# Performance work log

Hardware: AMD Instinct MI355X
Metric: run time of the kernel (lower is better)

The kernel has to match this reference:

```python
import jax, jax.numpy as jnp
import numpy as np

B, T, H = 512, 32, 300


def setup_inputs() -> dict:
    key = jax.random.key(0)
    ks = jax.random.split(key, 24)
    u = lambda k, shape: jax.random.uniform(k, shape, jnp.float32, -0.1, 0.1)
    return {
        'local_inputs': jax.random.normal(ks[0], (B, T, 28, 10), jnp.float32),
        'labels': jax.random.normal(ks[1], (B, T, 1, 1), jnp.float32),
        'extras': jax.random.normal(ks[2], (B, T, 4, 1), jnp.float32),
        'DisM': jax.random.normal(ks[3], (10,), jnp.float32),
        'AngleM': jax.random.uniform(ks[4], (10,), jnp.float32, 0.0, 360.0),
        'Wih': u(ks[5], (10, 4 * H, 11)),
        'b_ih': u(ks[6], (10, 4 * H)),
        'b_hh': u(ks[7], (10, 4 * H)),
        'Wt': u(ks[8], (4 * H, 4)),
        'bt_ih': u(ks[9], (4 * H,)),
        'bt_hh': u(ks[10], (4 * H,)),
        'wp': u(ks[11], (H, 2 * H)),
        'bp': u(ks[12], (H, 1)),
        'F1': u(ks[13], (2 * H, 200)),
        'b1': u(ks[14], (200,)),
        'F2': u(ks[15], (202, 1)),
        'b2': u(ks[16], (1,)),
        'ff': u(ks[17], (100, 17)),
        'bff': u(ks[18], (100, 1)),
        'fuse1': u(ks[19], (H, 100)),
        'biasf': u(ks[20], (100,)),
        'Wout': u(ks[21], (100, 1)),
        'biasout': u(ks[22], (1,)),
        'a': u(ks[23], (1,)),
    }


def reference(local_inputs, labels, extras, DisM, AngleM,
              Wih, b_ih, b_hh, Wt, bt_ih, bt_hh,
              wp, bp, F1, b1, F2, b2, ff, bff,
              fuse1, biasf, Wout, biasout, a):
    x = jnp.transpose(local_inputs, (1, 0, 2, 3))   # [T,B,28,10]
    exs = jnp.transpose(extras, (1, 0, 2, 3))       # [T,B,4,1]
    labels_r = jnp.transpose(labels, (1, 0, 2, 3)).reshape(T, B, 1)
    b_cells = b_ih + b_hh                            # weight_hh * 0 vanishes; biases remain
    bt = bt_ih + bt_hh
    wA = jax.nn.softmax(DisM)                        # [10] static distance weights
    aa = a[0]

    def cells(s):  # s: [B,11,10] -> con [B,H,10]; zero-state LSTMCell per neighbor
        g = jnp.einsum('kgi,bik->bkg', Wih, s) + b_cells  # [B,10,4H]
        i, f, gg, o = jnp.split(g, 4, axis=-1)
        h = jax.nn.sigmoid(o) * jnp.tanh(jax.nn.sigmoid(i) * jnp.tanh(gg))
        return jnp.transpose(h, (0, 2, 1))

    def target_cell(t):  # [B,4] -> [B,H]
        g = t @ Wt.T + bt
        i, f, gg, o = jnp.split(g, 4, axis=-1)
        return jax.nn.sigmoid(o) * jnp.tanh(jax.nn.sigmoid(i) * jnp.tanh(gg))

    def attend_predict(fl, con1, htarget):
        # fl: [B,28,10], con1: [B,H,10]
        hcat = jnp.concatenate([jnp.transpose(con1, (0, 2, 1)),
                                jnp.broadcast_to(htarget[:, None, :], (B, 10, H))], axis=2)  # [B,10,2H]
        fc1 = jax.nn.relu(jnp.einsum('bkh,ho->bko', hcat, F1) + b1)          # [B,10,200]
        ang = jnp.abs(fl[:, 10, :] - AngleM[None, :]) / 360.0                # [B,10]
        fc2 = jnp.concatenate([fc1, fl[:, 8, :, None], ang[..., None]], axis=2)  # [B,10,202]
        wdyn = jax.nn.relu(jnp.einsum('bko,od->bkd', fc2, F2)[..., 0] + b2[0])   # [B,10]
        # faithful to the original: softmax over neighbors of [10,B], then FLAT reshape to [B,1,10]
        wa3 = jax.nn.softmax(wdyn.T, axis=0).reshape(B, 1, 10)
        cat = jnp.sum(con1 * wa3, axis=2)                                    # [B,H]
        flin2 = jnp.einsum('of,bfk->bok', ff, fl[:, 11:, :]) + bff           # [B,100,10]
        fusiondis = jnp.sum(flin2 * wA[None, None, :], axis=2)               # [B,100]
        fuse = cat @ fuse1 + biasf                                           # [B,100]
        return (aa * fuse + (1.0 - aa) * fusiondis) @ Wout + biasout         # [B,1]

    # t = 0: con1 = con (no lastcon yet)
    con0 = cells(x[0, :, :11, :])
    p0 = attend_predict(x[0], con0, target_cell(exs[0, :, :4, 0]))

    def step(lastcon, inp):
        fl, e = inp
        con = cells(fl[:, :11, :])
        ht = target_cell(e[:, :4, 0])
        con1 = jax.nn.relu(jnp.einsum('oh,bhk->bok', wp,
                                      jnp.concatenate([con, lastcon], axis=1)) + bp)  # [B,H,10]
        return con, attend_predict(fl, con1, ht)

    _, preds = jax.lax.scan(step, con0, (x[1:], exs[1:]))
    preds = jnp.concatenate([p0[None], preds], axis=0)  # [T,B,1]
    return preds, labels_r
```

## Files before the change

kernel.cpp:

```cpp
#include <hip/hip_runtime.h>
#include <hip/hip_bf16.h>


#define TB 3
#define NBT 171
#define NR 32
#define NTHR 512
#define NW 8
#define KP 616
#define TBF 16

#define OFF_SM    0
#define OFF_WBF2  163840
#define OFF_F1S   256256
#define OFF_WCELL 319488
#define OFF_BTP   392448
#define OFF_WTP   393348
#define OFF_F1F   396948
#define OFF_WA    414868
#define OFF_SWA   414878
#define BASE_U32  414880
#define CON1_BYTE ((size_t)BASE_U32 * 4)
#define CONG_BYTE (CON1_BYTE + (size_t)98304000)
#define WS_NEED_BYTES (CONG_BYTE + (size_t)98304000)

typedef __attribute__((ext_vector_type(8))) short s16x8;
typedef __attribute__((ext_vector_type(4))) float f32x4;
typedef unsigned short u16;

__device__ __forceinline__ float rcpf(float x){ return __builtin_amdgcn_rcpf(x); }
__device__ __forceinline__ float sigf(float x){ return rcpf(1.0f+__expf(-x)); }
__device__ __forceinline__ float tanhf_(float x){ return 1.0f - 2.0f*rcpf(__expf(2.0f*x)+1.0f); }
__device__ __forceinline__ float bfu(u16 u){ return __uint_as_float(((unsigned)u)<<16); }
__device__ __forceinline__ u16 f2us(float f){ return (u16)(__float_as_uint(f)>>16); }
__device__ __forceinline__ u16 f2usr(float f){
  __hip_bfloat16 h = __float2bfloat16(f);
  return *(u16*)&h;
}

__global__ __launch_bounds__(256,4) void kern_cells(
    const float* __restrict__ li, const float* wsf, u16* __restrict__ cong)
{
  __shared__ __align__(16) float xs[64][12];
  const int tid=threadIdx.x;
  const int L = blockIdx.x + 10*blockIdx.y;
  const int virt = (L&7)*320 + (L>>3);
  const int k = virt%10;
  const int tbase = (virt/10)*64;
  const int t = tbase>>9, bg0 = tbase&511;
  for (int p=tid; p<64*11; p+=256){
    int r=p/11, i=p%11;
    xs[r][i] = li[(((size_t)(bg0+r)*32+t)*28+i)*10+k];
  }
  if (tid<64) xs[tid][11] = 1.0f;
  __syncthreads();
  const int w = tid>>6, lane = tid&63, lo=lane&15, qd=lane>>4;
  const int c4 = lane&3;
  short av[8];
  #pragma unroll
  for (int j=0;j<8;j++){
    int kk = qd*8+j;
    float v = (kk<12)? xs[w*16+lo][kk] : 0.f;
    av[j] = (short)f2usr(v);
  }
  s16x8 Ax = (s16x8){av[0],av[1],av[2],av[3],av[4],av[5],av[6],av[7]};
  const unsigned* wc = (const unsigned*)wsf + OFF_WCELL;
  const s16x8 Z = (s16x8){0,0,0,0,0,0,0,0};
  const size_t rowbase = ((size_t)(tbase + w*16 + qd*4 + c4)*10 + k)*300;
  for (int ht=0; ht<19; ht++){
    s16x8 Bi=Z, Bg=Z, Bo=Z;
    if (qd<2){
      const unsigned* bb = wc + (((k*19+ht)*3)*32 + qd*16+lo)*4;
      Bi = *(const s16x8*)(bb);
      Bg = *(const s16x8*)(bb + 32*4);
      Bo = *(const s16x8*)(bb + 64*4);
    }
    f32x4 gi={0.f,0.f,0.f,0.f}, gg={0.f,0.f,0.f,0.f}, go={0.f,0.f,0.f,0.f};
    gi = __builtin_amdgcn_mfma_f32_16x16x32_bf16(Ax, Bi, gi, 0,0,0);
    gg = __builtin_amdgcn_mfma_f32_16x16x32_bf16(Ax, Bg, gg, 0,0,0);
    go = __builtin_amdgcn_mfma_f32_16x16x32_bf16(Ax, Bo, go, 0,0,0);
    float v0 = sigf(go[0]) * tanhf_( sigf(gi[0]) * tanhf_(gg[0]) );
    float v1 = sigf(go[1]) * tanhf_( sigf(gi[1]) * tanhf_(gg[1]) );
    float v2 = sigf(go[2]) * tanhf_( sigf(gi[2]) * tanhf_(gg[2]) );
    float v3 = sigf(go[3]) * tanhf_( sigf(gi[3]) * tanhf_(gg[3]) );
    {
      bool hiC = (lane & 2) != 0;
      float s0 = hiC ? v0 : v2;
      float s1 = hiC ? v1 : v3;
      float r0 = __shfl_xor(s0, 2, 64);
      float r1 = __shfl_xor(s1, 2, 64);
      if (hiC){ v0 = r0; v1 = r1; } else { v2 = r0; v3 = r1; }
    }
    {
      bool odd = (lane & 1) != 0;
      float s0 = odd ? v0 : v1;
      float s1 = odd ? v2 : v3;
      float r0 = __shfl_xor(s0, 1, 64);
      float r1 = __shfl_xor(s1, 1, 64);
      if (odd){ v0 = r0; v2 = r1; } else { v1 = r0; v3 = r1; }
    }
    int g = (lane>>2)&3;
    if (!(ht==18 && g==3)){
      uint2 pk;
      pk.x = ((unsigned)f2usr(v1)<<16) | f2usr(v0);
      pk.y = ((unsigned)f2usr(v3)<<16) | f2usr(v2);
      *(uint2*)&cong[rowbase + ht*16 + 4*g] = pk;
    }
  }
}

__global__ __launch_bounds__(NTHR,8) void kern_main_split(
    const float* __restrict__ li, const float* __restrict__ exs,
    const float* __restrict__ AngleM, const float* __restrict__ bp,
    const float* __restrict__ F2, const float* __restrict__ b2,
    const float* wsf, unsigned* __restrict__ con1u, float* smg,
    const u16* __restrict__ cong)
{
  __shared__ __align__(16) u16 cct[NR][KP];
  __shared__ float xse[TB][2][10];
  __shared__ float exss[TB][4];
  __shared__ float wdP[NW][NR];
  __shared__ float wdL[NR];
  const int tid = threadIdx.x;
  const int L = blockIdx.x + NBT*blockIdx.y;
  const int virt = (L&7)*684 + (L>>3);
  const int bt = virt>>5, t = virt&31, b0 = bt*TB;
  const int w = tid>>6, lane = tid&63, lo = lane&15, qd = lane>>4;

  for (int p=tid;p<TB*20;p+=NTHR){
    int b=p/20, r=p%20, rr=r/10, k=r%10;
    int bg = b0+b; if (bg>511) bg=511;
    xse[b][rr][k] = li[((bg*32+t)*28 + (rr?10:8))*10 + k];
  }
  for (int p=tid;p<TB*4;p+=NTHR){
    int b=p/4, e=p%4;
    int bg = b0+b; if (bg>511) bg=511;
    exss[b][e] = exs[(bg*32+t)*4+e];
  }
  for (int p=tid; p<30*4; p+=NTHR){
    int n=p/4, c=p%4;
    ((unsigned*)&cct[n][600])[c] = 0u;
  }
  __syncthreads();

  const int nh = (t==0)?1:2;
  for (int p=tid; p<nh*TB*750; p+=NTHR){
    int half=p/(TB*750), r=p%(TB*750), n=r/75, op=r%75;
    int tp = half? t-1 : t;
    int bg = b0 + n/10; if (bg>511) bg=511;
    uint2 v = *(const uint2*)((const unsigned*)cong +
                ((size_t)(tp*512+bg)*10 + n%10)*150 + 2*op);
    *(uint2*)((unsigned*)&cct[n][300*half] + 2*op) = v;
  }
  __syncthreads();

  f32x4 acc[3][2];
  #pragma unroll
  for (int i=0;i<3;i++)
    #pragma unroll
    for (int nt=0;nt<2;nt++) acc[i][nt] = (f32x4){0.f,0.f,0.f,0.f};
  if (t>0){
    const u16* wbfA = (const u16*)((const unsigned*)wsf + OFF_WBF2);
    for (int ks=0; ks<19; ks++){
      const int kb = ks*32 + qd*8;
      s16x8 Bv[2];
      #pragma unroll
      for (int nt=0;nt<2;nt++)
        Bv[nt] = *(const s16x8*)&cct[nt*16+lo][kb];
      #pragma unroll
      for (int i=0;i<3;i++){
        int mt = i*8+w;
        if (mt<19){
          s16x8 Av = *(const s16x8*)(wbfA + ((size_t)(mt*19+ks)*64 + lane)*8);
          #pragma unroll
          for (int nt=0;nt<2;nt++)
            acc[i][nt] = __builtin_amdgcn_mfma_f32_16x16x32_bf16(Av, Bv[nt], acc[i][nt], 0,0,0);
        }
      }
    }
  }
  __syncthreads();

  if (t>0){
    #pragma unroll
    for (int i=0;i<3;i++){
      int mt = i*8+w;
      if (mt<19 && (mt<18 || qd<3)){
        int ob = mt*16 + qd*4;
        float p0=bp[ob], p1=bp[ob+1], p2=bp[ob+2], p3=bp[ob+3];
        #pragma unroll
        for (int nt=0;nt<2;nt++){
          int n = nt*16+lo;
          float v0=acc[i][nt][0]+p0, v1=acc[i][nt][1]+p1,
                v2=acc[i][nt][2]+p2, v3=acc[i][nt][3]+p3;
          unsigned w0 = ((unsigned)f2us(v1>0.f?v1:0.f)<<16) | f2us(v0>0.f?v0:0.f);
          unsigned w1 = ((unsigned)f2us(v3>0.f?v3:0.f)<<16) | f2us(v2>0.f?v2:0.f);
          *(unsigned*)&cct[n][ob]   = w0;
          *(unsigned*)&cct[n][ob+2] = w1;
        }
      }
    }
  }
  for (int p=tid; p<TB*75; p+=NTHR){
    int b=p/75, q=p%75, o=4*q;
    f32x4 ai={0.f,0.f,0.f,0.f}, ag={0.f,0.f,0.f,0.f}, ao={0.f,0.f,0.f,0.f};
    #pragma unroll
    for (int e=0;e<4;e++){
      float xv = exss[b][e];
      f32x4 wi = *(const f32x4*)&wsf[OFF_WTP+(e*3+0)*300+o];
      f32x4 wg = *(const f32x4*)&wsf[OFF_WTP+(e*3+1)*300+o];
      f32x4 wo = *(const f32x4*)&wsf[OFF_WTP+(e*3+2)*300+o];
      #pragma unroll
      for (int c=0;c<4;c++){
        ai[c] += wi[c]*xv; ag[c] += wg[c]*xv; ao[c] += wo[c]*xv;
      }
    }
    f32x4 bi = *(const f32x4*)&wsf[OFF_BTP+o];
    f32x4 bg = *(const f32x4*)&wsf[OFF_BTP+300+o];
    f32x4 bo = *(const f32x4*)&wsf[OFF_BTP+600+o];
    u16 u[4];
    #pragma unroll
    for (int c=0;c<4;c++){
      float vi = ai[c]+bi[c], vg = ag[c]+bg[c], vo = ao[c]+bo[c];
      u[c] = f2usr( sigf(vo)*tanhf_(sigf(vi)*tanhf_(vg)) );
    }
    uint2 pk;
    pk.x = ((unsigned)u[1]<<16) | u[0];
    pk.y = ((unsigned)u[3]<<16) | u[2];
    #pragma unroll
    for (int k=0;k<10;k++)
      *(uint2*)&cct[b*10+k][300+o] = pk;
  }
  for (int p=tid; p<30*4; p+=NTHR){
    int n=p/4, c=p%4;
    ((unsigned*)&cct[n][600])[c] = (c==0)? 0x00003f80u : 0u;
  }
  __syncthreads();

  for (int p=tid; p<TB*750; p+=NTHR){
    int n=p/75, op=p%75;
    int bg = b0 + n/10;
    if (bg < 512){
      uint2 v = *(const uint2*)((unsigned*)&cct[n][0] + 2*op);
      *(uint2*)(con1u + ((size_t)(t*512+bg)*10 + n%10)*150 + 2*op) = v;
    }
  }

  f32x4 acc2[2][2];
  #pragma unroll
  for (int mt=0;mt<2;mt++)
    #pragma unroll
    for (int j=0;j<2;j++) acc2[mt][j] = (f32x4){0.f,0.f,0.f,0.f};
  {
    const u16* f1s = (const u16*)((const unsigned*)wsf + OFF_F1S);
    for (int ks=0; ks<19; ks++){
      const int kb = ks*32 + qd*8;
      s16x8 Am[2];
      #pragma unroll
      for (int mt=0;mt<2;mt++)
        Am[mt] = *(const s16x8*)&cct[mt*16+lo][kb];
      #pragma unroll
      for (int j=0;j<2;j++){
        int nt = w + j*8;
        if (nt<13){
          s16x8 Bf = *(const s16x8*)(f1s + ((size_t)(nt*19+ks)*64 + lane)*8);
          #pragma unroll
          for (int mt=0;mt<2;mt++)
            acc2[mt][j] = __builtin_amdgcn_mfma_f32_16x16x32_bf16(Am[mt], Bf, acc2[mt][j], 0,0,0);
        }
      }
    }
  }
  {
    float f2c[2];
    #pragma unroll
    for (int j=0;j<2;j++){
      int nt = w + j*8;
      int jj = nt*16+lo;
      f2c[j] = (nt<13 && jj<200)? F2[jj] : 0.f;
    }
    #pragma unroll
    for (int mt=0;mt<2;mt++)
      #pragma unroll
      for (int r=0;r<4;r++){
        float s = 0.f;
        #pragma unroll
        for (int j=0;j<2;j++){
          float v = acc2[mt][j][r];
          s += (v>0.f? v:0.f) * f2c[j];
        }
        s += __shfl_xor(s,1,64); s += __shfl_xor(s,2,64);
        s += __shfl_xor(s,4,64); s += __shfl_xor(s,8,64);
        if (lo==0) wdP[w][mt*16+qd*4+r] = s;
      }
  }
  __syncthreads();
  if (tid<TB*10){
    int n=tid, b=n/10, k=n%10;
    float v = 0.f;
    #pragma unroll
    for (int ww=0;ww<NW;ww++) v += wdP[ww][n];
    float ang = fabsf(xse[b][1][k]-AngleM[k]) * (1.0f/360.0f);
    v += xse[b][0][k]*F2[200] + ang*F2[201] + b2[0];
    wdL[n] = v>0.f? v : 0.f;
  }
  __syncthreads();
  if (tid<TB && b0+tid < 512){
    int b=tid;
    float m = wdL[b*10];
    #pragma unroll
    for (int k=1;k<10;k++) m = fmaxf(m, wdL[b*10+k]);
    float e[10]; float s=0.f;
    #pragma unroll
    for (int k=0;k<10;k++){ e[k]=__expf(wdL[b*10+k]-m); s+=e[k]; }
    float inv = rcpf(s);
    #pragma unroll
    for (int k=0;k<10;k++) smg[t*5120 + k*512 + b0+b] = e[k]*inv;
  }
}

__global__ __launch_bounds__(NTHR,8) void kern_final(
    const float* __restrict__ li, const float* __restrict__ labels,
    const float* __restrict__ ff, const float* __restrict__ bff,
    const float* __restrict__ biasf, const float* __restrict__ Wout,
    const float* __restrict__ biasout, const float* __restrict__ a,
    const float* wsf, const unsigned* __restrict__ con1u,
    float* __restrict__ outp)
{
  __shared__ __align__(16) float cats[TBF][324];
  __shared__ __align__(16) float xs17[TBF][17][10];
  __shared__ float wa3s[TBF][10];
  __shared__ float dss[TBF][17];
  __shared__ float wAs[10];
  __shared__ float part[7][TBF];
  const int tid=threadIdx.x, t=blockIdx.y, bt=blockIdx.x, b0=bt*TBF;
  const int w = tid>>6, lane = tid&63, lo = lane&15, qd = lane>>4;
  if (tid>=NTHR-TBF){
    int b = tid-(NTHR-TBF);
    outp[16384 + t*512 + b0+b] = labels[(b0+b)*32+t];
  }
  for (int p=tid;p<TBF*85;p+=NTHR){
    int b=p/85, r=p%85, f=r/5, pr=r%5;
    *(float2*)&xs17[b][f][2*pr] =
        *(const float2*)&li[(((b0+b)*32+t)*28 + 11+f)*10 + 2*pr];
  }
  if (tid<10) wAs[tid] = wsf[OFF_WA+tid];
  for (int p=tid;p<TBF*10;p+=NTHR){
    int b=p/10, k=p%10;
    int g = (b0+b)*10+k;
    wa3s[b][k] = wsf[OFF_SM + t*5120 + (g>>9)*512 + (g&511)];
  }
  __syncthreads();
  for (int p=tid;p<TBF*17;p+=NTHR){
    int b=p/17, f=p%17; float s=0.f;
    #pragma unroll
    for (int k=0;k<10;k++) s += xs17[b][f][k]*wAs[k];
    dss[b][f]=s;
  }
  for (int p=tid;p<TBF*75;p+=NTHR){
    int b=p/75, q=p%75, o=4*q;
    const unsigned* base = con1u + ((size_t)(t*512 + b0+b)*10)*150 + 2*q;
    f32x4 s = {0.f,0.f,0.f,0.f};
    #pragma unroll
    for (int k=0;k<10;k++){
      uint2 cv = *(const uint2*)(base + (size_t)k*150);
      float wk = wa3s[b][k];
      s[0] += bfu((u16)(cv.x & 0xffffu))*wk;
      s[1] += bfu((u16)(cv.x >> 16))*wk;
      s[2] += bfu((u16)(cv.y & 0xffffu))*wk;
      s[3] += bfu((u16)(cv.y >> 16))*wk;
    }
    *(f32x4*)&cats[b][o] = s;
  }
  for (int p=tid;p<TBF*6;p+=NTHR){
    int b=p/6, c=p%6;
    *(f32x4*)&cats[b][300+4*c] = (f32x4){0.f,0.f,0.f,0.f};
  }
  __syncthreads();
  if (w < 7){
    f32x4 D = (f32x4){0.f,0.f,0.f,0.f};
    const u16* f1f = (const u16*)((const unsigned*)wsf + OFF_F1F);
    for (int ks=0; ks<10; ks++){
      const int kb = ks*32 + qd*8;
      f32x4 c0 = *(const f32x4*)&cats[lo][kb];
      f32x4 c1 = *(const f32x4*)&cats[lo][kb+4];
      short av[8];
      #pragma unroll
      for (int j=0;j<4;j++){
        av[j]   = (short)f2usr(c0[j]);
        av[4+j] = (short)f2usr(c1[j]);
      }
      s16x8 Ax = (s16x8){av[0],av[1],av[2],av[3],av[4],av[5],av[6],av[7]};
      s16x8 Bf = *(const s16x8*)(f1f + ((size_t)(w*10+ks)*64 + lane)*8);
      D = __builtin_amdgcn_mfma_f32_16x16x32_bf16(Ax, Bf, D, 0,0,0);
    }
    {
      int o = w*16+lo;
      bool ov = o<100;
      float aa = a[0], swa = wsf[OFF_SWA];
      float bfo = ov? biasf[o] : 0.f;
      float bffo = ov? bff[o]*swa : 0.f;
      float wo = ov? Wout[o] : 0.f;
      #pragma unroll
      for (int r=0;r<4;r++){
        int b = qd*4+r;
        float fu = D[r] + bfo;
        float fd = bffo;
        if (ov){
          #pragma unroll
          for (int f=0;f<17;f++) fd += ff[o*17+f]*dss[b][f];
        }
        float v = (aa*fu + (1.f-aa)*fd) * wo;
        v += __shfl_xor(v,1,64); v += __shfl_xor(v,2,64);
        v += __shfl_xor(v,4,64); v += __shfl_xor(v,8,64);
        if (lo==0) part[w][b] = v;
      }
    }
  }
  __syncthreads();
  if (tid<TBF){
    int b=tid;
    float v = biasout[0];
    #pragma unroll
    for (int ww=0;ww<7;ww++) v += part[ww][b];
    outp[t*512 + b0+b] = v;
  }
}

__global__ void kprep(const float* __restrict__ Wih, const float* __restrict__ b_ih,
                      const float* __restrict__ b_hh, const float* __restrict__ Wt,
                      const float* __restrict__ bt_ih, const float* __restrict__ bt_hh,
                      const float* __restrict__ wp, const float* __restrict__ F1,
                      const float* __restrict__ b1, const float* __restrict__ fuse1,
                      const float* __restrict__ DisM, float* __restrict__ wsf)
{
  int n = blockIdx.x*256 + threadIdx.x;
  if (n < 92416){
    int jp=n&3, lane=(n>>2)&63, rest=n>>8;
    int ks=rest%19, mt=rest/19;
    int m = mt*16 + (lane&15);
    int k = ks*32 + (lane>>4)*8 + 2*jp;
    float v0 = (m<300 && k  <600)? wp[m*600+k  ] : 0.f;
    float v1 = (m<300 && k+1<600)? wp[m*600+k+1] : 0.f;
    ((unsigned*)wsf)[OFF_WBF2+n] = ((unsigned)f2usr(v1)<<16) | f2usr(v0);
    return;
  }
  n -= 92416;
  if (n < 63232){
    int jp=n&3, lane=(n>>2)&63, rest=n>>8;
    int ks=rest%19, nt=rest/19;
    int col = nt*16 + (lane&15);
    int k = ks*32 + (lane>>4)*8 + 2*jp;
    float v0=0.f, v1=0.f;
    if (col<200){
      v0 = (k  <600)? F1[k*200+col]     : (k  ==600? b1[col] : 0.f);
      v1 = (k+1<600)? F1[(k+1)*200+col] : (k+1==600? b1[col] : 0.f);
    }
    ((unsigned*)wsf)[OFF_F1S+n] = ((unsigned)f2usr(v1)<<16) | f2usr(v0);
    return;
  }
  n -= 63232;
  if (n < 72960){
    int jp=n&3, l32=(n>>2)&31, rest=n>>7;
    int g=rest%3, rest2=rest/3, ht=rest2%19, k=rest2/19;
    int lo=l32&15, q16=l32>>4;
    int h = ht*16 + lo;
    int kk0 = q16*8 + 2*jp;
    float v0=0.f, v1=0.f;
    if (h < 300){
      int G = h + (g==0?0:(g==1?600:900));
      v0 = (kk0  <11)? Wih[(k*1200+G)*11+kk0]
         : (kk0 ==11? b_ih[k*1200+G]+b_hh[k*1200+G] : 0.f);
      int kk1 = kk0+1;
      v1 = (kk1  <11)? Wih[(k*1200+G)*11+kk1]
         : (kk1 ==11? b_ih[k*1200+G]+b_hh[k*1200+G] : 0.f);
    }
    ((unsigned*)wsf)[OFF_WCELL+n] = ((unsigned)f2usr(v1)<<16) | f2usr(v0);
    return;
  }
  n -= 72960;
  if (n < 900){
    int h=n%300, g=n/300;
    int G = h + (g==0?0:(g==1?600:900));
    wsf[OFF_BTP+n] = bt_ih[G]+bt_hh[G]; return;
  }
  n -= 900;
  if (n < 3600){
    int h=n%300; int q=n/300; int g=q%3, e=q/3;
    int G = h + (g==0?0:(g==1?600:900));
    wsf[OFF_WTP+n] = Wt[G*4+e]; return;
  }
  n -= 3600;
  if (n < 17920){
    int jp=n&3, lane=(n>>2)&63, rest=n>>8;
    int ks=rest%10, nt=rest/10;
    int col = nt*16 + (lane&15);
    int kk0 = ks*32 + (lane>>4)*8 + 2*jp;
    float v0 = (col<100 && kk0  <300)? fuse1[kk0*100+col]     : 0.f;
    float v1 = (col<100 && kk0+1<300)? fuse1[(kk0+1)*100+col] : 0.f;
    ((unsigned*)wsf)[OFF_F1F+n] = ((unsigned)f2usr(v1)<<16) | f2usr(v0);
    return;
  }
  n -= 17920;
  if (n == 0){
    float m = DisM[0];
    for (int k=1;k<10;k++) m = fmaxf(m, DisM[k]);
    float e[10]; float s=0.f;
    for (int k=0;k<10;k++){ e[k]=__expf(DisM[k]-m); s+=e[k]; }
    float inv=1.0f/s; float sw=0.f;
    for (int k=0;k<10;k++){ float v=e[k]*inv; wsf[OFF_WA+k]=v; sw+=v; }
    wsf[OFF_SWA]=sw;
  }
}

extern "C" void kernel_launch(void* const* d_in, const int* in_sizes, int n_in,
                              void* d_out, int out_size, void* d_ws, size_t ws_size,
                              hipStream_t stream)
{
  const float* li     = (const float*)d_in[0];
  const float* labels = (const float*)d_in[1];
  const float* exs    = (const float*)d_in[2];
  const float* DisM   = (const float*)d_in[3];
  const float* AngleM = (const float*)d_in[4];
  const float* Wih    = (const float*)d_in[5];
  const float* b_ih   = (const float*)d_in[6];
  const float* b_hh   = (const float*)d_in[7];
  const float* Wt     = (const float*)d_in[8];
  const float* bt_ih  = (const float*)d_in[9];
  const float* bt_hh  = (const float*)d_in[10];
  const float* wp     = (const float*)d_in[11];
  const float* bp     = (const float*)d_in[12];
  const float* F1     = (const float*)d_in[13];
  const float* b1     = (const float*)d_in[14];
  const float* F2     = (const float*)d_in[15];
  const float* b2     = (const float*)d_in[16];
  const float* ff     = (const float*)d_in[17];
  const float* bff    = (const float*)d_in[18];
  const float* fuse1  = (const float*)d_in[19];
  const float* biasf  = (const float*)d_in[20];
  const float* Wout   = (const float*)d_in[21];
  const float* biasout= (const float*)d_in[22];
  const float* a      = (const float*)d_in[23];
  float* wsf = (float*)d_ws;
  float* outp = (float*)d_out;
  unsigned* con1u = (unsigned*)((char*)d_ws + CON1_BYTE);
  u16* cong = (u16*)((char*)d_ws + CONG_BYTE);

  if (ws_size < WS_NEED_BYTES) return;

  kprep<<<dim3(981), dim3(256), 0, stream>>>(Wih,b_ih,b_hh,Wt,bt_ih,bt_hh,wp,F1,b1,fuse1,DisM,wsf);
  kern_cells<<<dim3(10,256), dim3(256), 0, stream>>>(li, wsf, cong);
  kern_main_split<<<dim3(NBT,32), NTHR, 0, stream>>>(li, exs, AngleM, bp, F2, b2,
                                                     wsf, con1u, wsf + OFF_SM, cong);
  kern_final<<<dim3(32,32), NTHR, 0, stream>>>(li, labels, ff, bff, biasf,
                                               Wout, biasout, a, wsf, con1u, outp);
}
```

Before: 377.4 us.

## Halve final-kernel batch tile, shrink block to 256 threads, trim main-kernel barriers

The final kernel now handles 8 batch rows per block with 256 threads and twice as many blocks. Each wave covers up to two output tiles, and half the MFMA A rows are zero-padded. In the main split kernel, one barrier between independent shared-memory fills is removed, and the last barrier is replaced by a single-wave lgkmcnt wait around the softmax tail. This aims to raise parallelism in the final stage and cut barrier overhead, at the cost of wasting half of each MFMA and relying on single-wave ordering for correctness.

```diff
diff --git a/kernel.cpp b/kernel.cpp
--- a/kernel.cpp
+++ b/kernel.cpp
@@ -8,7 +8,8 @@
 #define NTHR 512
 #define NW 8
 #define KP 616
-#define TBF 16
+#define TBF 8
+#define NTF 256
 
 #define OFF_SM    0
 #define OFF_WBF2  163840
@@ -141,7 +142,6 @@
     int n=p/4, c=p%4;
     ((unsigned*)&cct[n][600])[c] = 0u;
   }
-  __syncthreads();
 
   const int nh = (t==0)?1:2;
   for (int p=tid; p<nh*TB*750; p+=NTHR){
@@ -295,31 +295,33 @@
       }
   }
   __syncthreads();
-  if (tid<TB*10){
-    int n=tid, b=n/10, k=n%10;
-    float v = 0.f;
-    #pragma unroll
-    for (int ww=0;ww<NW;ww++) v += wdP[ww][n];
-    float ang = fabsf(xse[b][1][k]-AngleM[k]) * (1.0f/360.0f);
-    v += xse[b][0][k]*F2[200] + ang*F2[201] + b2[0];
-    wdL[n] = v>0.f? v : 0.f;
-  }
-  __syncthreads();
-  if (tid<TB && b0+tid < 512){
-    int b=tid;
-    float m = wdL[b*10];
-    #pragma unroll
-    for (int k=1;k<10;k++) m = fmaxf(m, wdL[b*10+k]);
-    float e[10]; float s=0.f;
-    #pragma unroll
-    for (int k=0;k<10;k++){ e[k]=__expf(wdL[b*10+k]-m); s+=e[k]; }
-    float inv = rcpf(s);
-    #pragma unroll
-    for (int k=0;k<10;k++) smg[t*5120 + k*512 + b0+b] = e[k]*inv;
+  if (tid < 64){
+    if (tid<TB*10){
+      int n=tid, b=n/10, k=n%10;
+      float v = 0.f;
+      #pragma unroll
+      for (int ww=0;ww<NW;ww++) v += wdP[ww][n];
+      float ang = fabsf(xse[b][1][k]-AngleM[k]) * (1.0f/360.0f);
+      v += xse[b][0][k]*F2[200] + ang*F2[201] + b2[0];
+      wdL[n] = v>0.f? v : 0.f;
+    }
+    asm volatile("s_waitcnt lgkmcnt(0)" ::: "memory");
+    if (tid<TB && b0+tid < 512){
+      int b=tid;
+      float m = wdL[b*10];
+      #pragma unroll
+      for (int k=1;k<10;k++) m = fmaxf(m, wdL[b*10+k]);
+      float e[10]; float s=0.f;
+      #pragma unroll
+      for (int k=0;k<10;k++){ e[k]=__expf(wdL[b*10+k]-m); s+=e[k]; }
+      float inv = rcpf(s);
+      #pragma unroll
+      for (int k=0;k<10;k++) smg[t*5120 + k*512 + b0+b] = e[k]*inv;
+    }
   }
 }
 
-__global__ __launch_bounds__(NTHR,8) void kern_final(
+__global__ __launch_bounds__(NTF,8) void kern_final(
     const float* __restrict__ li, const float* __restrict__ labels,
     const float* __restrict__ ff, const float* __restrict__ bff,
     const float* __restrict__ biasf, const float* __restrict__ Wout,
@@ -335,29 +337,29 @@
   __shared__ float part[7][TBF];
   const int tid=threadIdx.x, t=blockIdx.y, bt=blockIdx.x, b0=bt*TBF;
   const int w = tid>>6, lane = tid&63, lo = lane&15, qd = lane>>4;
-  if (tid>=NTHR-TBF){
-    int b = tid-(NTHR-TBF);
+  if (tid>=NTF-TBF){
+    int b = tid-(NTF-TBF);
     outp[16384 + t*512 + b0+b] = labels[(b0+b)*32+t];
   }
-  for (int p=tid;p<TBF*85;p+=NTHR){
+  for (int p=tid;p<TBF*85;p+=NTF){
     int b=p/85, r=p%85, f=r/5, pr=r%5;
     *(float2*)&xs17[b][f][2*pr] =
         *(const float2*)&li[(((b0+b)*32+t)*28 + 11+f)*10 + 2*pr];
   }
   if (tid<10) wAs[tid] = wsf[OFF_WA+tid];
-  for (int p=tid;p<TBF*10;p+=NTHR){
+  for (int p=tid;p<TBF*10;p+=NTF){
     int b=p/10, k=p%10;
     int g = (b0+b)*10+k;
     wa3s[b][k] = wsf[OFF_SM + t*5120 + (g>>9)*512 + (g&511)];
   }
   __syncthreads();
-  for (int p=tid;p<TBF*17;p+=NTHR){
+  for (int p=tid;p<TBF*17;p+=NTF){
     int b=p/17, f=p%17; float s=0.f;
     #pragma unroll
     for (int k=0;k<10;k++) s += xs17[b][f][k]*wAs[k];
     dss[b][f]=s;
   }
-  for (int p=tid;p<TBF*75;p+=NTHR){
+  for (int p=tid;p<TBF*75;p+=NTF){
     int b=p/75, q=p%75, o=4*q;
     const unsigned* base = con1u + ((size_t)(t*512 + b0+b)*10)*150 + 2*q;
     f32x4 s = {0.f,0.f,0.f,0.f};
@@ -372,48 +374,65 @@
     }
     *(f32x4*)&cats[b][o] = s;
   }
-  for (int p=tid;p<TBF*6;p+=NTHR){
+  for (int p=tid;p<TBF*6;p+=NTF){
     int b=p/6, c=p%6;
     *(f32x4*)&cats[b][300+4*c] = (f32x4){0.f,0.f,0.f,0.f};
   }
   __syncthreads();
-  if (w < 7){
-    f32x4 D = (f32x4){0.f,0.f,0.f,0.f};
+  {
+    f32x4 D[2] = {(f32x4){0.f,0.f,0.f,0.f}, (f32x4){0.f,0.f,0.f,0.f}};
     const u16* f1f = (const u16*)((const unsigned*)wsf + OFF_F1F);
     for (int ks=0; ks<10; ks++){
       const int kb = ks*32 + qd*8;
-      f32x4 c0 = *(const f32x4*)&cats[lo][kb];
-      f32x4 c1 = *(const f32x4*)&cats[lo][kb+4];
       short av[8];
-      #pragma unroll
-      for (int j=0;j<4;j++){
-        av[j]   = (short)f2usr(c0[j]);
-        av[4+j] = (short)f2usr(c1[j]);
+      if (lo < TBF){
+        f32x4 c0 = *(const f32x4*)&cats[lo][kb];
+        f32x4 c1 = *(const f32x4*)&cats[lo][kb+4];
+        #pragma unroll
+        for (int j=0;j<4;j++){
+          av[j]   = (short)f2usr(c0[j]);
+          av[4+j] = (short)f2usr(c1[j]);
+        }
+      } else {
+        #pragma unroll
+        for (int j=0;j<8;j++) av[j] = 0;
       }
       s16x8 Ax = (s16x8){av[0],av[1],av[2],av[3],av[4],av[5],av[6],av[7]};
-      s16x8 Bf = *(const s16x8*)(f1f + ((size_t)(w*10+ks)*64 + lane)*8);
-      D = __builtin_amdgcn_mfma_f32_16x16x32_bf16(Ax, Bf, D, 0,0,0);
-    }
-    {
-      int o = w*16+lo;
-      bool ov = o<100;
-      float aa = a[0], swa = wsf[OFF_SWA];
-      float bfo = ov? biasf[o] : 0.f;
-      float bffo = ov? bff[o]*swa : 0.f;
-      float wo = ov? Wout[o] : 0.f;
-      #pragma unroll
-      for (int r=0;r<4;r++){
-        int b = qd*4+r;
-        float fu = D[r] + bfo;
-        float fd = bffo;
-        if (ov){
-          #pragma unroll
-          for (int f=0;f<17;f++) fd += ff[o*17+f]*dss[b][f];
-        }
-        float v = (aa*fu + (1.f-aa)*fd) * wo;
-        v += __shfl_xor(v,1,64); v += __shfl_xor(v,2,64);
-        v += __shfl_xor(v,4,64); v += __shfl_xor(v,8,64);
-        if (lo==0) part[w][b] = v;
+      #pragma unroll
+      for (int j=0;j<2;j++){
+        int nt = w + j*4;
+        if (nt<7){
+          s16x8 Bf = *(const s16x8*)(f1f + ((size_t)(nt*10+ks)*64 + lane)*8);
+          D[j] = __builtin_amdgcn_mfma_f32_16x16x32_bf16(Ax, Bf, D[j], 0,0,0);
+        }
+      }
+    }
+    float aa = a[0], swa = wsf[OFF_SWA];
+    #pragma unroll
+    for (int j=0;j<2;j++){
+      int nt = w + j*4;
+      if (nt<7){
+        int o = nt*16+lo;
+        bool ov = o<100;
+        float bfo = ov? biasf[o] : 0.f;
+        float bffo = ov? bff[o]*swa : 0.f;
+        float wo = ov? Wout[o] : 0.f;
+        #pragma unroll
+        for (int r=0;r<4;r++){
+          int b = qd*4+r;
+          if (b < TBF){
+            float fu = D[j][r] + bfo;
+            float fd = bffo;
+            if (ov){
+              #pragma unroll
+              for (int f=0;f<17;f++) fd += ff[o*17+f]*dss[b][f];
+            }
+            float v = (aa*fu + (1.f-aa)*fd) * wo;
+            v += __shfl_xor(v,1,64); v += __shfl_xor(v,2,64);
+            v += __shfl_xor(v,4,64); v += __shfl_xor(v,8,64);
+            if (lo==0) part[nt][b] = v;
+          }
+        }
       }
     }
   }
@@ -552,6 +571,6 @@
   kern_cells<<<dim3(10,256), dim3(256), 0, stream>>>(li, wsf, cong);
   kern_main_split<<<dim3(NBT,32), NTHR, 0, stream>>>(li, exs, AngleM, bp, F2, b2,
                                                      wsf, con1u, wsf + OFF_SM, cong);
-  kern_final<<<dim3(32,32), NTHR, 0, stream>>>(li, labels, ff, bff, biasf,
-                                               Wout, biasout, a, wsf, con1u, outp);
+  kern_final<<<dim3(64,32), NTF, 0, stream>>>(li, labels, ff, bff, biasf,
+                                              Wout, biasout, a, wsf, con1u, outp);
 }
```

New measurement: 388.2 us. 1.03x slower.
